# Kernel tuning notes

Measured on AMD Instinct MI355X. Metric: run time of the kernel, lower is better.

The kernel has to match this reference:

```python
import jax, jax.numpy as jnp
import numpy as np

B, S, E, F, R, T = 2, 2048, 768, 3072, 4, 128
H = 12  # num_heads
HD = E // H
HID = 128  # lora_mlp_dim


def _lin(key, out_f, in_f):
    bound = 1.0 / np.sqrt(in_f)
    return jax.random.uniform(key, (out_f, in_f), jnp.float32, -bound, bound)


def _bias(key, out_f, in_f):
    bound = 1.0 / np.sqrt(in_f)
    return jax.random.uniform(key, (out_f,), jnp.float32, -bound, bound)


def setup_inputs() -> dict:
    key = jax.random.key(0)
    ks = jax.random.split(key, 20)
    return {
        "src": jax.random.normal(ks[0], (B, S, E), jnp.float32),
        "task_embedding": jax.random.normal(ks[1], (B, S, T), jnp.float32),
        "norm1_w": jnp.ones((E,), jnp.float32),
        "norm2_w": jnp.ones((E,), jnp.float32),
        "in_proj_w": _lin(ks[2], 3 * E, E),      # MHA qkv, bias=False
        "out_proj_w": _lin(ks[3], E, E),          # MHA out, bias=False
        "ffn1_w": _lin(ks[4], F, E), "ffn1_b": _bias(ks[5], F, E),
        "ffn2_w": _lin(ks[6], E, F), "ffn2_b": _bias(ks[7], E, F),
        "hA_w1": _lin(ks[8], HID, T), "hA_b1": _bias(ks[9], HID, T),
        "hA_w2": _lin(ks[10], F * R, HID), "hA_b2": _bias(ks[11], F * R, HID),
        "hB_w1": _lin(ks[12], HID, T), "hB_b1": _bias(ks[13], HID, T),
        "hB_w2": _lin(ks[14], R * E, HID), "hB_b2": _bias(ks[15], R * E, HID),
    }


def _rmsnorm(x, w):
    eps = jnp.finfo(x.dtype).eps
    return x * jax.lax.rsqrt(jnp.mean(x * x, axis=-1, keepdims=True) + eps) * w


def reference(src, task_embedding, norm1_w, norm2_w, in_proj_w, out_proj_w,
              ffn1_w, ffn1_b, ffn2_w, ffn2_b,
              hA_w1, hA_b1, hA_w2, hA_b2, hB_w1, hB_b1, hB_w2, hB_b2):
    # --- self-attention block (pre-RMSNorm) ---
    x = _rmsnorm(src, norm1_w)
    qkv = jnp.einsum('bse,fe->bsf', x, in_proj_w)  # [B,S,3E]
    q, k, v = jnp.split(qkv, 3, axis=-1)
    q = q.reshape(B, S, H, HD).transpose(0, 2, 1, 3)
    k = k.reshape(B, S, H, HD).transpose(0, 2, 1, 3)
    v = v.reshape(B, S, H, HD).transpose(0, 2, 1, 3)
    scores = jnp.einsum('bhqd,bhkd->bhqk', q, k) / jnp.sqrt(jnp.float32(HD))
    attn = jax.nn.softmax(scores, axis=-1)
    ctx = jnp.einsum('bhqk,bhkd->bhqd', attn, v)
    ctx = ctx.transpose(0, 2, 1, 3).reshape(B, S, E)
    attn_out = jnp.einsum('bse,fe->bsf', ctx, out_proj_w)
    src = src + attn_out

    # --- FFN block with per-token hypernetwork LoRA on linear1 ---
    x = _rmsnorm(src, norm2_w)
    # hypernetwork: MLP(task) -> per-token A [F,R], B [R,E]
    hA = jax.nn.relu(jnp.einsum('bst,ht->bsh', task_embedding, hA_w1) + hA_b1)
    A_params = (jnp.einsum('bsh,fh->bsf', hA, hA_w2) + hA_b2).reshape(B, S, F, R)
    hB = jax.nn.relu(jnp.einsum('bst,ht->bsh', task_embedding, hB_w1) + hB_b1)
    B_params = (jnp.einsum('bsh,fh->bsf', hB, hB_w2) + hB_b2).reshape(B, S, R, E)

    base = jnp.einsum('bse,fe->bsf', x, ffn1_w) + ffn1_b  # [B,S,F]
    inter = jnp.einsum('bse,bsre->bsr', x, B_params)       # [B,S,R]
    adapt = jnp.einsum('bsr,bsfr->bsf', inter, A_params)   # [B,S,F]
    h = jax.nn.relu(base + adapt)
    out2 = jnp.einsum('bsf,ef->bse', h, ffn2_w) + ffn2_b
    return src + out2
```

## Files before the change

### kernel.cpp

```cpp
#include <hip/hip_runtime.h>
#include <math.h>

#define NB 2
#define NS 2048
#define NE 768
#define NF 3072
#define NHEAD 12
#define NTOK 4096
#define LDW 1344
#define VTS 2176

typedef __bf16 bf16;
typedef __bf16 bf16x4 __attribute__((ext_vector_type(4)));
typedef __bf16 bf16x8 __attribute__((ext_vector_type(8)));
typedef float  f32x4  __attribute__((ext_vector_type(4)));

__device__ __forceinline__ f32x4 mfma_bf16(bf16x8 a, bf16x8 b, f32x4 c) {
  return __builtin_amdgcn_mfma_f32_16x16x32_bf16(a, b, c, 0, 0, 0);
}

__device__ __forceinline__ float fast_exp2(float x) {
#if __has_builtin(__builtin_amdgcn_exp2f)
  return __builtin_amdgcn_exp2f(x);
#else
  return exp2f(x);
#endif
}

__device__ __forceinline__ void glds16(const void* g, void* l) {
  __builtin_amdgcn_global_load_lds((const __attribute__((address_space(1))) void*)g,
                                   (__attribute__((address_space(3))) void*)l,
                                   16, 0, 0);
}

__device__ __forceinline__ void pipe_barrier_keep4() {
  asm volatile("s_waitcnt vmcnt(4)" ::: "memory");
  __builtin_amdgcn_s_barrier();
  __builtin_amdgcn_sched_barrier(0);
}
__device__ __forceinline__ void pipe_barrier_drain() {
  asm volatile("s_waitcnt vmcnt(0)" ::: "memory");
  __builtin_amdgcn_s_barrier();
  __builtin_amdgcn_sched_barrier(0);
}

__device__ __forceinline__ void swz_xy(int& bx, int& by) {
  int gx = gridDim.x;
  int i = by*gx + bx;
  int xcd = i & 7, s = i >> 3;
  int bands = gridDim.y >> 3;
  by = xcd*bands + s / gx;
  bx = s % gx;
}

__global__ void prep_kernel(const float* __restrict__ in_proj, const float* __restrict__ out_proj,
                            const float* __restrict__ ffn1_w, const float* __restrict__ ffn1_b,
                            const float* __restrict__ ffn2_w,
                            const float* __restrict__ hA_w1, const float* __restrict__ hA_b1,
                            const float* __restrict__ hA_w2, const float* __restrict__ hA_b2,
                            const float* __restrict__ hB_w1, const float* __restrict__ hB_b1,
                            const float* __restrict__ hB_w2,
                            const float* __restrict__ task,
                            bf16* __restrict__ Wqkv, bf16* __restrict__ Wo, bf16* __restrict__ W2,
                            bf16* __restrict__ W1ab, float* __restrict__ b1ab,
                            bf16* __restrict__ WBp, bf16* __restrict__ Wc,
                            bf16* __restrict__ task_bf)
{
  __shared__ float tb[64*130];
  int stride = gridDim.x * blockDim.x;
  int t0 = blockIdx.x * blockDim.x + threadIdx.x;
  const float QS = 0.125f * 1.44269504088896f;
  for (int i = t0; i < (2304*768)/4; i += stride) {
    float4 v = ((const float4*)in_proj)[i];
    float sc = (i < (768*768)/4) ? QS : 1.0f;
    *(bf16x4*)(Wqkv + i*4) = (bf16x4){(bf16)(v.x*sc), (bf16)(v.y*sc), (bf16)(v.z*sc), (bf16)(v.w*sc)};
  }
  for (int i = t0; i < (768*768)/4; i += stride) {
    float4 v = ((const float4*)out_proj)[i];
    *(bf16x4*)(Wo + i*4) = (bf16x4){(bf16)v.x, (bf16)v.y, (bf16)v.z, (bf16)v.w};
  }
  for (int i = t0; i < (768*3072)/4; i += stride) {
    float4 v = ((const float4*)ffn2_w)[i];
    *(bf16x4*)(W2 + i*4) = (bf16x4){(bf16)v.x, (bf16)v.y, (bf16)v.z, (bf16)v.w};
  }
  for (int i = t0; i < (NTOK*128)/4; i += stride) {
    float4 v = ((const float4*)task)[i];
    *(bf16x4*)(task_bf + i*4) = (bf16x4){(bf16)v.x, (bf16)v.y, (bf16)v.z, (bf16)v.w};
  }
  for (int i = t0; i < 256*128;  i += stride)
    W1ab[i] = (bf16)(i < 128*128 ? hA_w1[i] : hB_w1[i - 128*128]);
  for (int i = t0; i < 256; i += stride) b1ab[i] = (i < 128) ? hA_b1[i] : hB_b1[i-128];

  for (int j0 = blockIdx.x*64; j0 < 3072; j0 += gridDim.x*64) {
    __syncthreads();
    for (int i = threadIdx.x; i < 64*128; i += 256) {
      int jr = i >> 7, hh = i & 127;
      tb[jr*130 + hh] = hB_w2[(long)(j0 + jr)*128 + hh];
    }
    __syncthreads();
    int r = j0 / 768, e0 = j0 % 768;
    for (int i = threadIdx.x; i < 128*64; i += 256) {
      int hh = i >> 6, jr = i & 63;
      WBp[(long)(r*128 + hh)*768 + e0 + jr] = (bf16)tb[jr*130 + hh];
    }
  }

  for (int f = blockIdx.x; f < 3072; f += gridDim.x) {
    const float* hrow = hA_w2 + (long)f*512;
    bf16* wrow = Wc + (long)f*LDW;
    for (int c = threadIdx.x; c < 768; c += 256) wrow[c] = (bf16)ffn1_w[(long)f*768 + c];
    for (int i = threadIdx.x; i < 512; i += 256) {
      int r = i >> 7, h = i & 127;
      wrow[768 + h*4 + r] = (bf16)hrow[i];
    }
    if (threadIdx.x < 4)        wrow[1280 + threadIdx.x] = (bf16)hA_b2[f*4 + threadIdx.x];
    else if (threadIdx.x == 4)  wrow[1284] = (bf16)ffn1_b[f];
    else if (threadIdx.x < 64)  wrow[1280 + threadIdx.x] = (bf16)0.f;
  }
}

__global__ __launch_bounds__(256) void rmsnorm_k(const float* __restrict__ x,
                                                 const float* __restrict__ w,
                                                 bf16* __restrict__ out, int ld_out)
{
  __shared__ float red[4];
  long t = blockIdx.x;
  const float* xr = x + t*NE;
  float ss = 0.f;
  #pragma unroll
  for (int i = 0; i < 3; i++) { float v = xr[threadIdx.x + i*256]; ss += v*v; }
  #pragma unroll
  for (int d = 1; d < 64; d <<= 1) ss += __shfl_xor(ss, d, 64);
  if ((threadIdx.x & 63) == 0) red[threadIdx.x >> 6] = ss;
  __syncthreads();
  float tot = red[0] + red[1] + red[2] + red[3];
  float scale = rsqrtf(tot * (1.f/768.f) + 1.1920928955078125e-07f);
  #pragma unroll
  for (int i = 0; i < 3; i++) {
    int idx = threadIdx.x + i*256;
    out[t*ld_out + idx] = (bf16)(xr[idx] * scale * w[idx]);
  }
}

template<typename OutT, bool RELU, bool BIAS, bool RES>
__global__ __launch_bounds__(256) void gemm_bt_sw(const bf16* __restrict__ A,
                                                  const bf16* __restrict__ Bm,
                                                  OutT* __restrict__ C,
                                                  const float* __restrict__ bias,
                                                  const float* __restrict__ res,
                                                  int K, int lda, int ldb, int ldc)
{
  __shared__ bf16 As[3][128*32];
  __shared__ bf16 Bs[3][128*32];
  const int tid = threadIdx.x;
  int bx = blockIdx.x, by = blockIdx.y;
  swz_xy(bx, by);
  const int m0 = by * 128;
  const int n0 = bx * 128;
  const int w = tid >> 6, lane = tid & 63;
  const int quad = lane >> 4, l16 = lane & 15;
  const int wy = w >> 1, wx = w & 1;

  f32x4 acc[4][4];
  #pragma unroll
  for (int i = 0; i < 4; i++)
    #pragma unroll
    for (int j = 0; j < 4; j++) acc[i][j] = (f32x4){0.f,0.f,0.f,0.f};

  const int i0 = tid, i1 = tid + 256;
  const int R0 = i0 >> 3, cc0 = (i0 & 7) ^ (R0 & 7), r0 = 2*R0 + (cc0 >> 2), ch0 = (cc0 & 3) * 8;
  const int R1 = i1 >> 3, cc1 = (i1 & 7) ^ (R1 & 7), r1 = 2*R1 + (cc1 >> 2), ch1 = (cc1 & 3) * 8;
  const bf16* pA0 = A  + (long)(m0 + r0)*lda + ch0;
  const bf16* pA1 = A  + (long)(m0 + r1)*lda + ch1;
  const bf16* pB0 = Bm + (long)(n0 + r0)*ldb + ch0;
  const bf16* pB1 = Bm + (long)(n0 + r1)*ldb + ch1;
  auto stage = [&](int buf) {
    glds16(pA0, (void*)(&As[buf][i0*8]));
    glds16(pA1, (void*)(&As[buf][i1*8]));
    glds16(pB0, (void*)(&Bs[buf][i0*8]));
    glds16(pB1, (void*)(&Bs[buf][i1*8]));
    pA0 += 32; pA1 += 32; pB0 += 32; pB1 += 32;
  };

  stage(0);
  stage(1);
  pipe_barrier_keep4();

  const int Rh = l16 >> 1;
  const int ppq = ((l16 & 1) << 2) | quad;
  const int jfr = ppq ^ Rh;
  const int nsteps = K >> 5;
  int cur = 0, nx2 = 2;
  for (int s = 0; s < nsteps; ++s) {
    const bool more = (s + 2 < nsteps);
    if (more) stage(nx2);

    bf16x8 af[4], bfr[4];
    #pragma unroll
    for (int mi = 0; mi < 4; ++mi)
      af[mi] = *(const bf16x8*)(&As[cur][(wy*32 + mi*8 + Rh)*64 + jfr*8]);
    #pragma unroll
    for (int ni = 0; ni < 4; ++ni)
      bfr[ni] = *(const bf16x8*)(&Bs[cur][(wx*32 + ni*8 + Rh)*64 + jfr*8]);
    #pragma unroll
    for (int mi = 0; mi < 4; ++mi)
      #pragma unroll
      for (int ni = 0; ni < 4; ++ni)
        acc[mi][ni] = mfma_bf16(af[mi], bfr[ni], acc[mi][ni]);

    if (more) pipe_barrier_keep4();
    else      pipe_barrier_drain();
    cur = (cur == 2) ? 0 : cur + 1;
    nx2 = (nx2 == 2) ? 0 : nx2 + 1;
  }

  #pragma unroll
  for (int mi = 0; mi < 4; ++mi)
    #pragma unroll
    for (int ni = 0; ni < 4; ++ni) {
      int col = n0 + wx*64 + ni*16 + l16;
      #pragma unroll
      for (int r = 0; r < 4; ++r) {
        long row = m0 + wy*64 + mi*16 + quad*4 + r;
        float v = acc[mi][ni][r];
        if (BIAS) v += bias[col];
        if (RES)  v += res[row*ldc + col];
        if (RELU) v = v > 0.f ? v : 0.f;
        C[row*ldc + col] = (OutT)v;
      }
    }
}

template<typename OutT, bool RELU, bool BIAS, bool RES>
__global__ __launch_bounds__(256) void gemm64(const bf16* __restrict__ A,
                                              const bf16* __restrict__ Bm,
                                              OutT* __restrict__ C,
                                              const float* __restrict__ bias,
                                              const float* __restrict__ res,
                                              int K, int lda, int ldb, int ldc)
{
  __shared__ bf16 As[3][64*64];
  __shared__ bf16 Bs[3][64*64];
  const int tid = threadIdx.x;
  int bx = blockIdx.x, by = blockIdx.y;
  swz_xy(bx, by);
  const int m0 = by * 64, n0 = bx * 64;
  const int w = tid >> 6, lane = tid & 63;
  const int quad = lane >> 4, l16 = lane & 15;
  const int wy = w >> 1, wx = w & 1;
  const int sw = l16 & 7;

  f32x4 acc[2][2];
  #pragma unroll
  for (int i = 0; i < 2; i++)
    #pragma unroll
    for (int j = 0; j < 2; j++) acc[i][j] = (f32x4){0.f,0.f,0.f,0.f};

  const int c0 = tid, c1 = tid + 256;
  const int r0 = c0 >> 3, g0 = ((c0 & 7) ^ (r0 & 7)) * 8;
  const int r1 = c1 >> 3, g1 = ((c1 & 7) ^ (r1 & 7)) * 8;
  const bf16* pA0 = A  + (long)(m0 + r0)*lda + g0;
  const bf16* pA1 = A  + (long)(m0 + r1)*lda + g1;
  const bf16* pB0 = Bm + (long)(n0 + r0)*ldb + g0;
  const bf16* pB1 = Bm + (long)(n0 + r1)*ldb + g1;
  auto stage = [&](int buf) {
    glds16(pA0, (void*)(&As[buf][c0*8]));
    glds16(pA1, (void*)(&As[buf][c1*8]));
    glds16(pB0, (void*)(&Bs[buf][c0*8]));
    glds16(pB1, (void*)(&Bs[buf][c1*8]));
    pA0 += 64; pA1 += 64; pB0 += 64; pB1 += 64;
  };

  const int nsteps = K >> 6;
  stage(0);
  if (nsteps > 1) stage(1);
  pipe_barrier_keep4();

  int cur = 0, nx2 = 2;
  for (int s = 0; s < nsteps; ++s) {
    const bool more = (s + 2 < nsteps);
    if (more) stage(nx2);

    bf16x8 af[2][2], bfr[2][2];
    #pragma unroll
    for (int mi = 0; mi < 2; ++mi)
      #pragma unroll
      for (int kb = 0; kb < 2; ++kb)
        af[mi][kb] = *(const bf16x8*)(&As[cur][(wy*32 + mi*16 + l16)*64 + (((kb*4 + quad) ^ sw))*8]);
    #pragma unroll
    for (int ni = 0; ni < 2; ++ni)
      #pragma unroll
      for (int kb = 0; kb < 2; ++kb)
        bfr[ni][kb] = *(const bf16x8*)(&Bs[cur][(wx*32 + ni*16 + l16)*64 + (((kb*4 + quad) ^ sw))*8]);
    #pragma unroll
    for (int kb = 0; kb < 2; ++kb)
      #pragma unroll
      for (int mi = 0; mi < 2; ++mi)
        #pragma unroll
        for (int ni = 0; ni < 2; ++ni)
          acc[mi][ni] = mfma_bf16(af[mi][kb], bfr[ni][kb], acc[mi][ni]);

    if (more) pipe_barrier_keep4();
    else      pipe_barrier_drain();
    cur = (cur == 2) ? 0 : cur + 1;
    nx2 = (nx2 == 2) ? 0 : nx2 + 1;
  }

  #pragma unroll
  for (int mi = 0; mi < 2; ++mi)
    #pragma unroll
    for (int ni = 0; ni < 2; ++ni) {
      int col = n0 + wx*32 + ni*16 + l16;
      #pragma unroll
      for (int r = 0; r < 4; ++r) {
        long row = m0 + wy*32 + mi*16 + quad*4 + r;
        float v = acc[mi][ni][r];
        if (BIAS) v += bias[col];
        if (RES)  v += res[row*ldc + col];
        if (RELU) v = v > 0.f ? v : 0.f;
        C[row*ldc + col] = (OutT)v;
      }
    }
}

__global__ __launch_bounds__(256) void gemm_qkv64(const bf16* __restrict__ A,
                                                  const bf16* __restrict__ Bm,
                                                  bf16* __restrict__ Qkv,
                                                  bf16* __restrict__ Vt)
{
  __shared__ bf16 As[3][64*64];
  __shared__ bf16 Bs[3][64*64];
  const int tid = threadIdx.x;
  int bx = blockIdx.x, by = blockIdx.y;
  swz_xy(bx, by);
  const int m0 = by * 64, n0 = bx * 64;
  const int w = tid >> 6, lane = tid & 63;
  const int quad = lane >> 4, l16 = lane & 15;
  const int wy = w >> 1, wx = w & 1;
  const int sw = l16 & 7;

  f32x4 acc[2][2];
  #pragma unroll
  for (int i = 0; i < 2; i++)
    #pragma unroll
    for (int j = 0; j < 2; j++) acc[i][j] = (f32x4){0.f,0.f,0.f,0.f};

  const int c0 = tid, c1 = tid + 256;
  const int r0 = c0 >> 3, g0 = ((c0 & 7) ^ (r0 & 7)) * 8;
  const int r1 = c1 >> 3, g1 = ((c1 & 7) ^ (r1 & 7)) * 8;
  const bf16* pA0 = A  + (long)(m0 + r0)*768 + g0;
  const bf16* pA1 = A  + (long)(m0 + r1)*768 + g1;
  const bf16* pB0 = Bm + (long)(n0 + r0)*768 + g0;
  const bf16* pB1 = Bm + (long)(n0 + r1)*768 + g1;
  auto stage = [&](int buf) {
    glds16(pA0, (void*)(&As[buf][c0*8]));
    glds16(pA1, (void*)(&As[buf][c1*8]));
    glds16(pB0, (void*)(&Bs[buf][c0*8]));
    glds16(pB1, (void*)(&Bs[buf][c1*8]));
    pA0 += 64; pA1 += 64; pB0 += 64; pB1 += 64;
  };

  stage(0);
  stage(1);
  pipe_barrier_keep4();

  int cur = 0, nx2 = 2;
  for (int s = 0; s < 12; ++s) {
    const bool more = (s + 2 < 12);
    if (more) stage(nx2);

    bf16x8 af[2][2], bfr[2][2];
    #pragma unroll
    for (int mi = 0; mi < 2; ++mi)
      #pragma unroll
      for (int kb = 0; kb < 2; ++kb)
        af[mi][kb] = *(const bf16x8*)(&As[cur][(wy*32 + mi*16 + l16)*64 + (((kb*4 + quad) ^ sw))*8]);
    #pragma unroll
    for (int ni = 0; ni < 2; ++ni)
      #pragma unroll
      for (int kb = 0; kb < 2; ++kb)
        bfr[ni][kb] = *(const bf16x8*)(&Bs[cur][(wx*32 + ni*16 + l16)*64 + (((kb*4 + quad) ^ sw))*8]);
    #pragma unroll
    for (int kb = 0; kb < 2; ++kb)
      #pragma unroll
      for (int mi = 0; mi < 2; ++mi)
        #pragma unroll
        for (int ni = 0; ni < 2; ++ni)
          acc[mi][ni] = mfma_bf16(af[mi][kb], bfr[ni][kb], acc[mi][ni]);

    if (more) pipe_barrier_keep4();
    else      pipe_barrier_drain();
    cur = (cur == 2) ? 0 : cur + 1;
    nx2 = (nx2 == 2) ? 0 : nx2 + 1;
  }

  const int bb = m0 >> 11;
  #pragma unroll
  for (int mi = 0; mi < 2; ++mi)
    #pragma unroll
    for (int ni = 0; ni < 2; ++ni) {
      int col = n0 + wx*32 + ni*16 + l16;
      #pragma unroll
      for (int r = 0; r < 4; ++r) {
        long row = m0 + wy*32 + mi*16 + quad*4 + r;
        bf16 v = (bf16)acc[mi][ni][r];
        if (col < 1536) {
          Qkv[row*2304 + col] = v;
        } else {
          int vc = col - 1536;
          int hh = vc >> 6, d = vc & 63;
          long srow = row & (NS-1);
          Vt[((long)(bb*NHEAD + hh)*64 + d)*VTS + srow] = v;
        }
      }
    }
}

__global__ __launch_bounds__(256, 2) void flash_attn(const bf16* __restrict__ Qkv,
                                                     const bf16* __restrict__ Vt,
                                                     bf16* __restrict__ Ctx)
{
  __shared__ bf16 Ks[2][2][64*64];
  __shared__ bf16 Vs[2][2][64*64];

  const int tid = threadIdx.x;
  const int w = tid >> 6, lane = tid & 63;
  const int quad = lane >> 4, l16 = lane & 15;
  const int pair = w >> 1, qw = w & 1;
  int bx = blockIdx.x, by = blockIdx.y;
  swz_xy(bx, by);
  const int bh = by;
  const int b = bh / NHEAD, h = bh % NHEAD;
  const int q0 = bx * 64;

  bf16x8 qf[2][2];
  #pragma unroll
  for (int mi = 0; mi < 2; ++mi) {
    const long tq = (long)(b*NS + q0 + qw*32 + mi*16 + l16);
    qf[mi][0] = *(const bf16x8*)(Qkv + tq*2304 + h*64 + quad*8);
    qf[mi][1] = *(const bf16x8*)(Qkv + tq*2304 + h*64 + 32 + quad*8);
  }

  bf16x8 ones;
  #pragma unroll
  for (int j = 0; j < 8; ++j) ones[j] = (bf16)1.0f;

  f32x4 o[2][4];
  f32x4 o5[2];
  #pragma unroll
  for (int mi = 0; mi < 2; ++mi) {
    o5[mi] = (f32x4){0.f,0.f,0.f,0.f};
    #pragma unroll
    for (int i = 0; i < 4; i++) o[mi][i] = (f32x4){0.f,0.f,0.f,0.f};
  }

  const int ptid = tid & 127;
  const bf16* kp[4];
  const bf16* vp[4];
  int cc[4];
  #pragma unroll
  for (int i = 0; i < 4; ++i) {
    int c = ptid + i*128;
    cc[i] = c;
    int r = c >> 3, g = ((c & 7) ^ (r & 7)) * 8;
    kp[i] = Qkv + (long)(b*NS + pair*1024 + r)*2304 + 768 + h*64 + g;
    vp[i] = Vt + ((long)bh*64 + r)*VTS + pair*1024 + g;
  }
  auto stage = [&](int buf) {
    #pragma unroll
    for (int i = 0; i < 4; ++i) {
      glds16(kp[i], (void*)(&Ks[pair][buf][cc[i]*8]));
      glds16(vp[i], (void*)(&Vs[pair][buf][cc[i]*8]));
      kp[i] += (long)64*2304; vp[i] += 64;
    }
  };

  auto body = [&](int cur) {
    bf16x8 kfr[4][2];
    #pragma unroll
    for (int nt = 0; nt < 4; ++nt)
      #pragma unroll
      for (int kb = 0; kb < 2; ++kb)
        kfr[nt][kb] = *(const bf16x8*)(&Ks[pair][cur][(nt*16 + l16)*64 + (((kb*4 + quad) ^ (l16 & 7)))*8]);

    bf16x8 pf[2][2];
    #pragma unroll
    for (int mi = 0; mi < 2; ++mi) {
      f32x4 s[4];
      #pragma unroll
      for (int nt = 0; nt < 4; ++nt) {
        s[nt] = (f32x4){0.f,0.f,0.f,0.f};
        #pragma unroll
        for (int kb = 0; kb < 2; ++kb)
          s[nt] = mfma_bf16(kfr[nt][kb], qf[mi][kb], s[nt]);
      }
      #pragma unroll
      for (int nt = 0; nt < 4; ++nt)
        #pragma unroll
        for (int r = 0; r < 4; ++r)
          pf[mi][nt >> 1][(nt & 1)*4 + r] = (bf16)fast_exp2(s[nt][r]);
    }
    #pragma unroll
    for (int ntp = 0; ntp < 2; ++ntp) {
      bf16x8 vf[4];
      #pragma unroll
      for (int dt = 0; dt < 4; ++dt) {
        int row = dt*16 + l16;
        int cA = ntp*4 + (quad >> 1);
        int base = row*64 + (quad & 1)*4;
        bf16x4 va = *(const bf16x4*)(&Vs[pair][cur][base + ((cA       ^ (row & 7)) << 3)]);
        bf16x4 vb = *(const bf16x4*)(&Vs[pair][cur][base + (((cA + 2) ^ (row & 7)) << 3)]);
        vf[dt] = (bf16x8){va[0],va[1],va[2],va[3], vb[0],vb[1],vb[2],vb[3]};
      }
      #pragma unroll
      for (int mi = 0; mi < 2; ++mi) {
        #pragma unroll
        for (int dt = 0; dt < 4; ++dt)
          o[mi][dt] = mfma_bf16(pf[mi][ntp], vf[dt], o[mi][dt]);
        o5[mi] = mfma_bf16(pf[mi][ntp], ones, o5[mi]);
      }
    }
  };

  stage(0);
  __builtin_amdgcn_s_waitcnt(0);
  __syncthreads();

  for (int t = 0; t < 16; t += 2) {
    stage(1);
    body(0);
    __builtin_amdgcn_s_waitcnt(0);
    __syncthreads();
    if (t + 2 < 16) stage(0);
    body(1);
    __builtin_amdgcn_s_waitcnt(0);
    __syncthreads();
  }

  float* Of = (float*)&Ks[0][0][0];
  float* Lf = Of + 64*68;
  const int rbase = qw*32;
  if (pair == 1) {
    #pragma unroll
    for (int mi = 0; mi < 2; ++mi)
      #pragma unroll
      for (int r = 0; r < 4; ++r) {
        int row = rbase + mi*16 + quad*4 + r;
        if (l16 == 0) Lf[row] = o5[mi][r];
        #pragma unroll
        for (int dt = 0; dt < 4; ++dt)
          Of[row*68 + dt*16 + l16] = o[mi][dt][r];
      }
  }
  __syncthreads();
  if (pair == 0) {
    #pragma unroll
    for (int mi = 0; mi < 2; ++mi)
      #pragma unroll
      for (int r = 0; r < 4; ++r) {
        int row = rbase + mi*16 + quad*4 + r;
        float inv = 1.f / (o5[mi][r] + Lf[row]);
        long trow = (long)(b*NS + q0 + row);
        #pragma unroll
        for (int dt = 0; dt < 4; ++dt)
          Ctx[trow*NE + h*64 + dt*16 + l16] =
            (bf16)((o[mi][dt][r] + Of[row*68 + dt*16 + l16]) * inv);
      }
  }
}

__global__ __launch_bounds__(256) void build_g(const bf16* __restrict__ HAB,
                                               const float* __restrict__ P,
                                               const float* __restrict__ hB_b2,
                                               bf16* __restrict__ Aext)
{
  long t = blockIdx.x*4 + (threadIdx.x >> 6);
  int lane = threadIdx.x & 63;
  const bf16* xr = Aext + t*LDW;
  float acc[4] = {0.f, 0.f, 0.f, 0.f};
  for (int i = lane; i < 768; i += 64) {
    float xv = (float)xr[i];
    #pragma unroll
    for (int r = 0; r < 4; ++r) acc[r] += xv * hB_b2[r*768 + i];
  }
  const bf16* hB = HAB + t*256 + 128;
  const float* Pr = P + t*512;
  #pragma unroll
  for (int k = 0; k < 2; ++k) {
    int h = lane + k*64;
    float hv = (float)hB[h];
    #pragma unroll
    for (int r = 0; r < 4; ++r) acc[r] += hv * Pr[r*128 + h];
  }
  #pragma unroll
  for (int r = 0; r < 4; ++r)
    #pragma unroll
    for (int d = 1; d < 64; d <<= 1) acc[r] += __shfl_xor(acc[r], d, 64);

  bf16* grow = Aext + t*LDW + 768;
  const bf16* hA = HAB + t*256;
  #pragma unroll
  for (int j = 0; j < 8; ++j) {
    int idx = lane*8 + j;
    int h = idx >> 2, r = idx & 3;
    grow[idx] = (bf16)((float)hA[h] * acc[r]);
  }
  if (lane < 4)       Aext[t*LDW + 1280 + lane] = (bf16)acc[lane];
  else if (lane == 4) Aext[t*LDW + 1284] = (bf16)1.0f;
  else                Aext[t*LDW + 1280 + lane] = (bf16)0.f;
}

extern "C" void kernel_launch(void* const* d_in, const int* in_sizes, int n_in,
                              void* d_out, int out_size, void* d_ws, size_t ws_size,
                              hipStream_t stream)
{
  const float* src      = (const float*)d_in[0];
  const float* task     = (const float*)d_in[1];
  const float* norm1_w  = (const float*)d_in[2];
  const float* norm2_w  = (const float*)d_in[3];
  const float* in_proj  = (const float*)d_in[4];
  const float* out_proj = (const float*)d_in[5];
  const float* ffn1_w   = (const float*)d_in[6];
  const float* ffn1_b   = (const float*)d_in[7];
  const float* ffn2_w   = (const float*)d_in[8];
  const float* ffn2_b   = (const float*)d_in[9];
  const float* hA_w1    = (const float*)d_in[10];
  const float* hA_b1    = (const float*)d_in[11];
  const float* hA_w2    = (const float*)d_in[12];
  const float* hA_b2    = (const float*)d_in[13];
  const float* hB_w1    = (const float*)d_in[14];
  const float* hB_b1    = (const float*)d_in[15];
  const float* hB_w2    = (const float*)d_in[16];
  const float* hB_b2    = (const float*)d_in[17];
  float* out = (float*)d_out;

  char* ws = (char*)d_ws;
  size_t off = 0;
  auto alloc = [&](size_t bytes) { size_t o = off; off += (bytes + 255) & ~(size_t)255; return o; };
  bf16*  Wqkv   = (bf16*)(ws + alloc(2304*768*2));
  bf16*  Wo     = (bf16*)(ws + alloc(768*768*2));
  bf16*  W2     = (bf16*)(ws + alloc(768*3072*2));
  bf16*  W1ab   = (bf16*)(ws + alloc(256*128*2));
  float* b1ab   = (float*)(ws + alloc(256*4));
  bf16*  WBp    = (bf16*)(ws + alloc(512*768*2));
  bf16*  Wc     = (bf16*)(ws + alloc((size_t)3072*LDW*2));
  bf16*  taskbf = (bf16*)(ws + alloc((size_t)NTOK*128*2));
  bf16*  XC     = (bf16*)(ws + alloc((size_t)NTOK*768*2));
  char*  QKVH   = ws + alloc(25559040);
  bf16*  Qkv    = (bf16*)QKVH;
  bf16*  Vt     = (bf16*)(QKVH + 18874368);
  bf16*  Hbuf   = (bf16*)QKVH;
  float* Src2   = (float*)(ws + alloc((size_t)NTOK*768*4));
  bf16*  Aext   = (bf16*)(ws + alloc((size_t)NTOK*LDW*2));
  bf16*  HAB    = (bf16*)(ws + alloc((size_t)NTOK*256*2));
  float* P      = (float*)(ws + alloc((size_t)NTOK*512*4));

  prep_kernel<<<dim3(1280), 256, 0, stream>>>(in_proj, out_proj, ffn1_w, ffn1_b, ffn2_w,
      hA_w1, hA_b1, hA_w2, hA_b2, hB_w1, hB_b1, hB_w2, task,
      Wqkv, Wo, W2, W1ab, b1ab, WBp, Wc, taskbf);
  rmsnorm_k<<<dim3(NTOK), 256, 0, stream>>>(src, norm1_w, XC, 768);
  gemm_qkv64<<<dim3(36,64), 256, 0, stream>>>(XC, Wqkv, Qkv, Vt);
  flash_attn<<<dim3(32,24), 256, 0, stream>>>(Qkv, Vt, XC);
  gemm64<float,false,false,true><<<dim3(12,64), 256, 0, stream>>>(XC, Wo, Src2, nullptr, src, 768, 768, 768, 768);
  rmsnorm_k<<<dim3(NTOK), 256, 0, stream>>>(Src2, norm2_w, Aext, LDW);
  gemm64<bf16,true,true,false><<<dim3(4,64), 256, 0, stream>>>(taskbf, W1ab, HAB, b1ab, nullptr, 128, 128, 128, 256);
  gemm64<float,false,false,false><<<dim3(8,64), 256, 0, stream>>>(Aext, WBp, P, nullptr, nullptr, 768, LDW, 768, 512);
  build_g<<<dim3(NTOK/4), 256, 0, stream>>>(HAB, P, hB_b2, Aext);
  gemm_bt_sw<bf16,true,false,false><<<dim3(24,32), 256, 0, stream>>>(Aext, Wc, Hbuf, nullptr, nullptr, 1312, LDW, LDW, 3072);
  gemm64<float,false,true,true><<<dim3(12,64), 256, 0, stream>>>(Hbuf, W2, out, ffn2_b, Src2, 3072, 3072, 3072, 768);
}
```

Measured before the change: 212.5 us.

## Use 128x128 tiles for QKV projection GEMM and raise attention MFMA priority

Replaces the 64x64-tile QKV GEMM with a 128x128-tile version using a 32-wide K step, a new swizzled shared-memory layout and a 4x4 MFMA accumulator grid per wave. Larger tiles raise arithmetic intensity and cut redundant global loads, at the cost of fewer blocks (576 vs 2304) and more registers per thread. Separately, the flash-attention compute body is wrapped in s_setprio so its waves get issue priority over load-issuing waves.

```diff
diff --git a/kernel.cpp b/kernel.cpp
--- a/kernel.cpp
+++ b/kernel.cpp
@@ -231,6 +231,96 @@
     }
 }
 
+__global__ __launch_bounds__(256) void gemm_qkv128(const bf16* __restrict__ A,
+                                                   const bf16* __restrict__ Bm,
+                                                   bf16* __restrict__ Qkv,
+                                                   bf16* __restrict__ Vt)
+{
+  __shared__ bf16 As[3][128*32];
+  __shared__ bf16 Bs[3][128*32];
+  const int tid = threadIdx.x;
+  int bx = blockIdx.x, by = blockIdx.y;
+  swz_xy(bx, by);
+  const int m0 = by * 128;
+  const int n0 = bx * 128;
+  const int w = tid >> 6, lane = tid & 63;
+  const int quad = lane >> 4, l16 = lane & 15;
+  const int wy = w >> 1, wx = w & 1;
+
+  f32x4 acc[4][4];
+  #pragma unroll
+  for (int i = 0; i < 4; i++)
+    #pragma unroll
+    for (int j = 0; j < 4; j++) acc[i][j] = (f32x4){0.f,0.f,0.f,0.f};
+
+  const int i0 = tid, i1 = tid + 256;
+  const int R0 = i0 >> 3, cc0 = (i0 & 7) ^ (R0 & 7), r0 = 2*R0 + (cc0 >> 2), ch0 = (cc0 & 3) * 8;
+  const int R1 = i1 >> 3, cc1 = (i1 & 7) ^ (R1 & 7), r1 = 2*R1 + (cc1 >> 2), ch1 = (cc1 & 3) * 8;
+  const bf16* pA0 = A  + (long)(m0 + r0)*768 + ch0;
+  const bf16* pA1 = A  + (long)(m0 + r1)*768 + ch1;
+  const bf16* pB0 = Bm + (long)(n0 + r0)*768 + ch0;
+  const bf16* pB1 = Bm + (long)(n0 + r1)*768 + ch1;
+  auto stage = [&](int buf) {
+    glds16(pA0, (void*)(&As[buf][i0*8]));
+    glds16(pA1, (void*)(&As[buf][i1*8]));
+    glds16(pB0, (void*)(&Bs[buf][i0*8]));
+    glds16(pB1, (void*)(&Bs[buf][i1*8]));
+    pA0 += 32; pA1 += 32; pB0 += 32; pB1 += 32;
+  };
+
+  stage(0);
+  stage(1);
+  pipe_barrier_keep4();
+
+  const int Rh = l16 >> 1;
+  const int ppq = ((l16 & 1) << 2) | quad;
+  const int jfr = ppq ^ Rh;
+  int cur = 0, nx2 = 2;
+  for (int s = 0; s < 24; ++s) {
+    const bool more = (s + 2 < 24);
+    if (more) stage(nx2);
+
+    bf16x8 af[4], bfr[4];
+    #pragma unroll
+    for (int mi = 0; mi < 4; ++mi)
+      af[mi] = *(const bf16x8*)(&As[cur][(wy*32 + mi*8 + Rh)*64 + jfr*8]);
+    #pragma unroll
+    for (int ni = 0; ni < 4; ++ni)
+      bfr[ni] = *(const bf16x8*)(&Bs[cur][(wx*32 + ni*8 + Rh)*64 + jfr*8]);
+    #pragma unroll
+    for (int mi = 0; mi < 4; ++mi)
+      #pragma unroll
+      for (int ni = 0; ni < 4; ++ni)
+        acc[mi][ni] = mfma_bf16(af[mi], bfr[ni], acc[mi][ni]);
+
+    if (more) pipe_barrier_keep4();
+    else      pipe_barrier_drain();
+    cur = (cur == 2) ? 0 : cur + 1;
+    nx2 = (nx2 == 2) ? 0 : nx2 + 1;
+  }
+
+  #pragma unroll
+  for (int mi = 0; mi < 4; ++mi)
+    #pragma unroll
+    for (int ni = 0; ni < 4; ++ni) {
+      int col = n0 + wx*64 + ni*16 + l16;
+      #pragma unroll
+      for (int r = 0; r < 4; ++r) {
+        long row = m0 + wy*64 + mi*16 + quad*4 + r;
+        bf16 v = (bf16)acc[mi][ni][r];
+        if (col < 1536) {
+          Qkv[row*2304 + col] = v;
+        } else {
+          int vc = col - 1536;
+          int hh = vc >> 6, d = vc & 63;
+          long bb = row >> 11;
+          long srow = row & (NS-1);
+          Vt[((bb*NHEAD + hh)*64 + d)*VTS + srow] = v;
+        }
+      }
+    }
+}
+
 template<typename OutT, bool RELU, bool BIAS, bool RES>
 __global__ __launch_bounds__(256) void gemm64(const bf16* __restrict__ A,
                                               const bf16* __restrict__ Bm,
@@ -323,99 +413,6 @@
     }
 }
 
-__global__ __launch_bounds__(256) void gemm_qkv64(const bf16* __restrict__ A,
-                                                  const bf16* __restrict__ Bm,
-                                                  bf16* __restrict__ Qkv,
-                                                  bf16* __restrict__ Vt)
-{
-  __shared__ bf16 As[3][64*64];
-  __shared__ bf16 Bs[3][64*64];
-  const int tid = threadIdx.x;
-  int bx = blockIdx.x, by = blockIdx.y;
-  swz_xy(bx, by);
-  const int m0 = by * 64, n0 = bx * 64;
-  const int w = tid >> 6, lane = tid & 63;
-  const int quad = lane >> 4, l16 = lane & 15;
-  const int wy = w >> 1, wx = w & 1;
-  const int sw = l16 & 7;
-
-  f32x4 acc[2][2];
-  #pragma unroll
-  for (int i = 0; i < 2; i++)
-    #pragma unroll
-    for (int j = 0; j < 2; j++) acc[i][j] = (f32x4){0.f,0.f,0.f,0.f};
-
-  const int c0 = tid, c1 = tid + 256;
-  const int r0 = c0 >> 3, g0 = ((c0 & 7) ^ (r0 & 7)) * 8;
-  const int r1 = c1 >> 3, g1 = ((c1 & 7) ^ (r1 & 7)) * 8;
-  const bf16* pA0 = A  + (long)(m0 + r0)*768 + g0;
-  const bf16* pA1 = A  + (long)(m0 + r1)*768 + g1;
-  const bf16* pB0 = Bm + (long)(n0 + r0)*768 + g0;
-  const bf16* pB1 = Bm + (long)(n0 + r1)*768 + g1;
-  auto stage = [&](int buf) {
-    glds16(pA0, (void*)(&As[buf][c0*8]));
-    glds16(pA1, (void*)(&As[buf][c1*8]));
-    glds16(pB0, (void*)(&Bs[buf][c0*8]));
-    glds16(pB1, (void*)(&Bs[buf][c1*8]));
-    pA0 += 64; pA1 += 64; pB0 += 64; pB1 += 64;
-  };
-
-  stage(0);
-  stage(1);
-  pipe_barrier_keep4();
-
-  int cur = 0, nx2 = 2;
-  for (int s = 0; s < 12; ++s) {
-    const bool more = (s + 2 < 12);
-    if (more) stage(nx2);
-
-    bf16x8 af[2][2], bfr[2][2];
-    #pragma unroll
-    for (int mi = 0; mi < 2; ++mi)
-      #pragma unroll
-      for (int kb = 0; kb < 2; ++kb)
-        af[mi][kb] = *(const bf16x8*)(&As[cur][(wy*32 + mi*16 + l16)*64 + (((kb*4 + quad) ^ sw))*8]);
-    #pragma unroll
-    for (int ni = 0; ni < 2; ++ni)
-      #pragma unroll
-      for (int kb = 0; kb < 2; ++kb)
-        bfr[ni][kb] = *(const bf16x8*)(&Bs[cur][(wx*32 + ni*16 + l16)*64 + (((kb*4 + quad) ^ sw))*8]);
-    #pragma unroll
-    for (int kb = 0; kb < 2; ++kb)
-      #pragma unroll
-      for (int mi = 0; mi < 2; ++mi)
-        #pragma unroll
-        for (int ni = 0; ni < 2; ++ni)
-          acc[mi][ni] = mfma_bf16(af[mi][kb], bfr[ni][kb], acc[mi][ni]);
-
-    if (more) pipe_barrier_keep4();
-    else      pipe_barrier_drain();
-    cur = (cur == 2) ? 0 : cur + 1;
-    nx2 = (nx2 == 2) ? 0 : nx2 + 1;
-  }
-
-  const int bb = m0 >> 11;
-  #pragma unroll
-  for (int mi = 0; mi < 2; ++mi)
-    #pragma unroll
-    for (int ni = 0; ni < 2; ++ni) {
-      int col = n0 + wx*32 + ni*16 + l16;
-      #pragma unroll
-      for (int r = 0; r < 4; ++r) {
-        long row = m0 + wy*32 + mi*16 + quad*4 + r;
-        bf16 v = (bf16)acc[mi][ni][r];
-        if (col < 1536) {
-          Qkv[row*2304 + col] = v;
-        } else {
-          int vc = col - 1536;
-          int hh = vc >> 6, d = vc & 63;
-          long srow = row & (NS-1);
-          Vt[((long)(bb*NHEAD + hh)*64 + d)*VTS + srow] = v;
-        }
-      }
-    }
-}
-
 __global__ __launch_bounds__(256, 2) void flash_attn(const bf16* __restrict__ Qkv,
                                                      const bf16* __restrict__ Vt,
                                                      bf16* __restrict__ Ctx)
@@ -476,6 +473,7 @@
   };
 
   auto body = [&](int cur) {
+    __builtin_amdgcn_s_setprio(1);
     bf16x8 kfr[4][2];
     #pragma unroll
     for (int nt = 0; nt < 4; ++nt)
@@ -520,6 +518,7 @@
         o5[mi] = mfma_bf16(pf[mi][ntp], ones, o5[mi]);
       }
     }
+    __builtin_amdgcn_s_setprio(0);
   };
 
   stage(0);
@@ -659,7 +658,7 @@
       hA_w1, hA_b1, hA_w2, hA_b2, hB_w1, hB_b1, hB_w2, task,
       Wqkv, Wo, W2, W1ab, b1ab, WBp, Wc, taskbf);
   rmsnorm_k<<<dim3(NTOK), 256, 0, stream>>>(src, norm1_w, XC, 768);
-  gemm_qkv64<<<dim3(36,64), 256, 0, stream>>>(XC, Wqkv, Qkv, Vt);
+  gemm_qkv128<<<dim3(18,32), 256, 0, stream>>>(XC, Wqkv, Qkv, Vt);
   flash_attn<<<dim3(32,24), 256, 0, stream>>>(Qkv, Vt, XC);
   gemm64<float,false,false,true><<<dim3(12,64), 256, 0, stream>>>(XC, Wo, Src2, nullptr, src, 768, 768, 768, 768);
   rmsnorm_k<<<dim3(NTOK), 256, 0, stream>>>(Src2, norm2_w, Aext, LDW);
```

After: 213.8 us. No clear change (+0.6%).
